# Optimization experiments

Hardware: AMD Instinct MI355X
Metric: run time of the kernel (lower is better)

## Reference

```python
import jax, jax.numpy as jnp
import numpy as np

N_NODES = 100000


def _gcn_conv(h, src, dst, norm, W, b, n):
    # linear transform then symmetric-normalized scatter-add aggregation
    hw = h @ W                                   # [N, out]
    msg = hw[src] * norm[:, None]                # [E+N, out] gathered messages
    out = jax.ops.segment_sum(msg, dst, num_segments=n)
    return out + b


def _self_loops_and_norm(edge_index, n):
    loop = jnp.arange(n, dtype=edge_index.dtype)
    src = jnp.concatenate([edge_index[0], loop])
    dst = jnp.concatenate([edge_index[1], loop])
    deg = jax.ops.segment_sum(jnp.ones_like(src, dtype=jnp.float32), dst, num_segments=n)
    dinv = jnp.where(deg > 0, jax.lax.rsqrt(jnp.maximum(deg, 1.0)), 0.0)
    norm = dinv[src] * dinv[dst]                 # D^-1/2 (A+I) D^-1/2 coefficients
    return src, dst, norm


def setup_inputs() -> dict:
    key = jax.random.key(0)
    k1, k2, k3, k4 = jax.random.split(key, 4)
    F_IN, H, C = 128, 64, 40
    x = jax.random.normal(k1, (N_NODES, F_IN), dtype=jnp.float32)
    edge_index = jax.random.randint(k2, (2, 3200000), 0, N_NODES, dtype=jnp.int64)
    s1 = 1.0 / np.sqrt(F_IN)
    s2 = 1.0 / np.sqrt(H)
    W1 = jax.random.uniform(k3, (F_IN, H), jnp.float32, -s1, s1)
    b1 = jnp.zeros((H,), jnp.float32)
    W2 = jax.random.uniform(k4, (H, C), jnp.float32, -s2, s2)
    b2 = jnp.zeros((C,), jnp.float32)
    return {"x": x, "edge_index": edge_index, "W1": W1, "b1": b1, "W2": W2, "b2": b2}


def reference(x, edge_index, W1, b1, W2, b2):
    n = x.shape[0]
    src, dst, norm = _self_loops_and_norm(edge_index, n)
    h = _gcn_conv(x, src, dst, norm, W1, b1, n)
    h = jax.nn.relu(h)
    # dropout(p=0.5) is identity in eval mode
    out = _gcn_conv(h, src, dst, norm, W2, b2, n)
    return jax.nn.log_softmax(out, axis=1)
```

## Files before the change

kernel.cpp:

```cpp
#include <hip/hip_runtime.h>
#include <math.h>

#define F_IN 128
#define HID  64
#define NCLS 40
#define PART_CHUNK 4096
#define CAP 4608
#define MAXNB 1024
#define ASTRIDE 132

typedef _Float16 half8 __attribute__((ext_vector_type(8)));
typedef _Float16 half2t __attribute__((ext_vector_type(2)));
typedef float floatx4 __attribute__((ext_vector_type(4)));

__device__ inline half8 ld_half8_u8(const _Float16* p) {
    union { uint2 u[2]; half8 h; } r;
    r.u[0] = *(const uint2*)p;
    r.u[1] = *(const uint2*)(p + 4);
    return r.h;
}

__global__ __launch_bounds__(256) void fused_part_gemm1(const int* __restrict__ src,
                                                        const int* __restrict__ dst,
                                                        int* __restrict__ bCur,
                                                        int* __restrict__ pkBuf,
                                                        int E, int NB, int nPart,
                                                        const float* __restrict__ x,
                                                        const float* __restrict__ W1,
                                                        _Float16* __restrict__ h1, int n) {
    __shared__ __align__(16) char smem[2 * 64 * ASTRIDE * 2];
    int tid = threadIdx.x;
    if ((int)blockIdx.x < nPart) {
        int* hcnt  = (int*)smem;
        int* hbase = (int*)smem + MAXNB;
        for (int i = tid; i < NB; i += 256) hcnt[i] = 0;
        __syncthreads();
        int e0 = blockIdx.x * PART_CHUNK;
        int s_[16], d_[16];
#pragma unroll
        for (int i = 0; i < 16; ++i) {
            int e = e0 + i * 256 + tid;
            if (e < E) {
                s_[i] = src[e]; d_[i] = dst[e];
                atomicAdd(&hcnt[d_[i] >> 7], 1);
            }
        }
        __syncthreads();
        for (int b = tid; b < NB; b += 256) {
            int c = hcnt[b];
            hbase[b] = c ? (b * CAP + atomicAdd(&bCur[b], c)) : 0;
            hcnt[b] = 0;
        }
        __syncthreads();
#pragma unroll
        for (int i = 0; i < 16; ++i) {
            int e = e0 + i * 256 + tid;
            if (e < E) {
                int b = d_[i] >> 7;
                int loc = atomicAdd(&hcnt[b], 1);
                pkBuf[hbase[b] + loc] = (s_[i] << 7) | (d_[i] & 127);
            }
        }
    } else {
        _Float16* Ah = (_Float16*)smem;
        _Float16* Wt = Ah + 64 * ASTRIDE;
        int node0 = ((int)blockIdx.x - nPart) * 64;
#pragma unroll
        for (int i = 0; i < 8; ++i) {
            int f = (i * 256 + tid) * 4;
            int m = f >> 7, k = f & 127;
            float4 v = (node0 + m < n) ? ((const float4*)(x + (size_t)(node0 + m) * F_IN))[k >> 2]
                                       : make_float4(0.f, 0.f, 0.f, 0.f);
            _Float16* p = &Ah[m * ASTRIDE + k];
            p[0] = (_Float16)v.x; p[1] = (_Float16)v.y; p[2] = (_Float16)v.z; p[3] = (_Float16)v.w;
        }
#pragma unroll
        for (int i = 0; i < 32; ++i) {
            int f = i * 256 + tid;
            int k = f >> 6, nn = f & 63;
            Wt[nn * ASTRIDE + k] = (_Float16)W1[f];
        }
        __syncthreads();
        int wave = tid >> 6, lane = tid & 63;
        int m0 = wave * 16;
        int col = lane & 15, quad = lane >> 4;
        floatx4 acc[4] = {{0,0,0,0},{0,0,0,0},{0,0,0,0},{0,0,0,0}};
#pragma unroll
        for (int kk = 0; kk < 4; ++kk) {
            int kbase = kk * 32 + quad * 8;
            half8 a = ld_half8_u8(&Ah[(m0 + col) * ASTRIDE + kbase]);
#pragma unroll
            for (int t = 0; t < 4; ++t) {
                half8 b = ld_half8_u8(&Wt[(t * 16 + col) * ASTRIDE + kbase]);
                acc[t] = __builtin_amdgcn_mfma_f32_16x16x32_f16(a, b, acc[t], 0, 0, 0);
            }
        }
#pragma unroll
        for (int t = 0; t < 4; ++t)
#pragma unroll
            for (int r = 0; r < 4; ++r) {
                int node = node0 + m0 + quad * 4 + r;
                if (node < n) h1[(size_t)node * HID + t * 16 + col] = (_Float16)acc[t][r];
            }
    }
}

__global__ __launch_bounds__(256) void scan_buckets(const int* __restrict__ bCur,
                                                    int* __restrict__ bBase, int NB, int E) {
    __shared__ int part[256];
    int tid = threadIdx.x;
    int v[4]; int sum = 0;
#pragma unroll
    for (int k = 0; k < 4; ++k) {
        int i = tid * 4 + k;
        v[k] = (i < NB) ? bCur[i] : 0;
        sum += v[k];
    }
    part[tid] = sum; __syncthreads();
    for (int off = 1; off < 256; off <<= 1) {
        int t = (tid >= off) ? part[tid - off] : 0;
        __syncthreads();
        part[tid] += t;
        __syncthreads();
    }
    int base = part[tid] - sum;
#pragma unroll
    for (int k = 0; k < 4; ++k) {
        int i = tid * 4 + k;
        if (i < NB) bBase[i] = base;
        base += v[k];
    }
    if (tid == 255) bBase[NB] = E;
}

__global__ __launch_bounds__(256) void bucket_finalize(const int* __restrict__ bCur,
                                                       const int* __restrict__ bBase,
                                                       const int* __restrict__ pkBuf,
                                                       int* __restrict__ ptr,
                                                       float* __restrict__ dinv,
                                                       int* __restrict__ sIdx, int n, int E) {
    __shared__ int cnt128[128];
    __shared__ int sc[128];
    __shared__ int cur[128];
    int b = blockIdx.x;
    int node0 = b << 7;
    int tid = threadIdx.x;
    if (tid < 128) cnt128[tid] = 0;
    __syncthreads();
    int beg = b * CAP, end = beg + bCur[b];
    int dbase = bBase[b];
    for (int j = beg + tid; j < end; j += 256)
        atomicAdd(&cnt128[pkBuf[j] & 127], 1);
    __syncthreads();
    int v = (tid < 128) ? cnt128[tid] : 0;
    if (tid < 128) sc[tid] = v;
    __syncthreads();
    for (int off = 1; off < 128; off <<= 1) {
        int t = (tid < 128 && tid >= off) ? sc[tid - off] : 0;
        __syncthreads();
        if (tid < 128) sc[tid] += t;
        __syncthreads();
    }
    if (tid < 128) {
        int node = node0 + tid;
        if (node < n) {
            int p = dbase + sc[tid] - v;
            ptr[node] = p;
            cur[tid] = p;
            dinv[node] = rsqrtf((float)v + 1.0f);
        }
    }
    if (tid == 0 && b == gridDim.x - 1) ptr[n] = E;
    __syncthreads();
    for (int j = beg + tid; j < end; j += 256) {
        int p = pkBuf[j];
        int pos = atomicAdd(&cur[p & 127], 1);
        sIdx[pos] = p >> 7;
    }
}

template<bool RELU>
__global__ __launch_bounds__(256) void gather4(const int* __restrict__ ptr,
                                               const int* __restrict__ sIdx,
                                               const float* __restrict__ dinv,
                                               const _Float16* __restrict__ hin,
                                               const float* __restrict__ bias,
                                               _Float16* __restrict__ hout, int n) {
    int tid = threadIdx.x, wave = tid >> 6, lane = tid & 63;
    int ng   = lane >> 4;
    int slot = (lane >> 3) & 1;
    int fq   = lane & 7;
    int node = blockIdx.x * 16 + wave * 4 + ng;
    bool valid = node < n;
    int nodeC = valid ? node : 0;
    int beg = ptr[nodeC];
    int end = valid ? ptr[nodeC + 1] : beg;
    float di = dinv[nodeC];
    float a0[8] = {0,0,0,0,0,0,0,0}, a1[8] = {0,0,0,0,0,0,0,0};

    if (slot == 0 && valid) {
        half8 v = *(const half8*)(hin + nodeC * HID + fq * 8);
        float w = di * di;
#pragma unroll
        for (int j = 0; j < 8; ++j) a0[j] = (float)v[j] * w;
    }
    for (int j0 = beg; j0 < end; j0 += 8) {
        int ja = j0 + slot, jb = j0 + 2 + slot, jc = j0 + 4 + slot, jd = j0 + 6 + slot;
        bool va = ja < end, vb = jb < end, vc = jc < end, vd = jd < end;
        int sa = sIdx[va ? ja : beg];
        int sb = sIdx[vb ? jb : beg];
        int sc_ = sIdx[vc ? jc : beg];
        int sd = sIdx[vd ? jd : beg];
        float wa = va ? dinv[sa] * di : 0.f;
        float wb = vb ? dinv[sb] * di : 0.f;
        float wc = vc ? dinv[sc_] * di : 0.f;
        float wd = vd ? dinv[sd] * di : 0.f;
        half8 ra = *(const half8*)(hin + sa * HID + fq * 8);
        half8 rb = *(const half8*)(hin + sb * HID + fq * 8);
        half8 rc = *(const half8*)(hin + sc_ * HID + fq * 8);
        half8 rd = *(const half8*)(hin + sd * HID + fq * 8);
#if __has_builtin(__builtin_amdgcn_fdot2)
        half2t wab = { (_Float16)wa, (_Float16)wb };
        half2t wcd = { (_Float16)wc, (_Float16)wd };
#pragma unroll
        for (int j = 0; j < 8; ++j) {
            half2t pab = { ra[j], rb[j] };
            half2t pcd = { rc[j], rd[j] };
            a0[j] = __builtin_amdgcn_fdot2(pab, wab, a0[j], false);
            a1[j] = __builtin_amdgcn_fdot2(pcd, wcd, a1[j], false);
        }
#else
#pragma unroll
        for (int j = 0; j < 8; ++j) {
            a0[j] = fmaf((float)ra[j], wa, a0[j]);
            a0[j] = fmaf((float)rb[j], wb, a0[j]);
            a1[j] = fmaf((float)rc[j], wc, a1[j]);
            a1[j] = fmaf((float)rd[j], wd, a1[j]);
        }
#endif
    }
#pragma unroll
    for (int j = 0; j < 8; ++j) {
        a0[j] += a1[j];
        a0[j] += __shfl_xor(a0[j], 8, 64);
    }
    if (slot == 0 && valid) {
        union { half8 h; uint4 u; } o;
#pragma unroll
        for (int j = 0; j < 8; ++j) {
            float v = a0[j];
            if (RELU) v = fmaxf(v + bias[fq * 8 + j], 0.f);
            o.h[j] = (_Float16)v;
        }
        *(uint4*)(hout + nodeC * HID + fq * 8) = o.u;
    }
}

#define GSTRIDE 72
__global__ __launch_bounds__(256) void gemm2_mfma_logsm(const _Float16* __restrict__ g,
                                                        const float* __restrict__ W2,
                                                        const float* __restrict__ b2,
                                                        float* __restrict__ out, int n) {
    __shared__ _Float16 gt[64 * GSTRIDE];
    __shared__ _Float16 wt[48 * GSTRIDE];
    int tid = threadIdx.x;
    int node0 = blockIdx.x * 64;
#pragma unroll
    for (int i = 0; i < 2; ++i) {
        int f = (i * 256 + tid) * 8;
        int m = f >> 6, k = f & 63;
        union { uint4 u; half8 h; } v;
        if (node0 + m < n) v.u = *(const uint4*)(g + (size_t)(node0 + m) * HID + k);
        else v.u = make_uint4(0, 0, 0, 0);
        *(uint4*)&gt[m * GSTRIDE + k] = v.u;
    }
#pragma unroll
    for (int i = 0; i < 12; ++i) {
        int f = i * 256 + tid;
        int c = f >> 6, k = f & 63;
        wt[c * GSTRIDE + k] = (c < NCLS) ? (_Float16)W2[k * NCLS + c] : (_Float16)0.f;
    }
    __syncthreads();

    int wave = tid >> 6, lane = tid & 63;
    int m0 = wave * 16;
    int col = lane & 15, quad = lane >> 4;
    floatx4 acc[3] = {{0,0,0,0},{0,0,0,0},{0,0,0,0}};
#pragma unroll
    for (int kk = 0; kk < 2; ++kk) {
        int kbase = kk * 32 + quad * 8;
        half8 a = *(const half8*)&gt[(m0 + col) * GSTRIDE + kbase];
#pragma unroll
        for (int t = 0; t < 3; ++t) {
            half8 b = *(const half8*)&wt[(t * 16 + col) * GSTRIDE + kbase];
            acc[t] = __builtin_amdgcn_mfma_f32_16x16x32_f16(a, b, acc[t], 0, 0, 0);
        }
    }
    float bb[3];
#pragma unroll
    for (int t = 0; t < 3; ++t) {
        int c = t * 16 + col;
        bb[t] = (c < NCLS) ? b2[c] : 0.f;
    }
#pragma unroll
    for (int r = 0; r < 4; ++r) {
        int node = node0 + m0 + quad * 4 + r;
        float v0 = acc[0][r] + bb[0];
        float v1 = acc[1][r] + bb[1];
        float v2 = (col < 8) ? acc[2][r] + bb[2] : -INFINITY;
        float m = fmaxf(fmaxf(v0, v1), v2);
#pragma unroll
        for (int off = 1; off < 16; off <<= 1) m = fmaxf(m, __shfl_xor(m, off, 64));
        float s = expf(v0 - m) + expf(v1 - m) + ((col < 8) ? expf(v2 - m) : 0.f);
#pragma unroll
        for (int off = 1; off < 16; off <<= 1) s += __shfl_xor(s, off, 64);
        float ls = logf(s);
        if (node < n) {
            float* op = out + (size_t)node * NCLS;
            op[col]      = v0 - m - ls;
            op[16 + col] = v1 - m - ls;
            if (col < 8) op[32 + col] = v2 - m - ls;
        }
    }
}

extern "C" void kernel_launch(void* const* d_in, const int* in_sizes, int n_in,
                              void* d_out, int out_size, void* d_ws, size_t ws_size,
                              hipStream_t stream) {
    const float* x  = (const float*)d_in[0];
    const int*   ei = (const int*)d_in[1];
    const float* W1 = (const float*)d_in[2];
    const float* b1 = (const float*)d_in[3];
    const float* W2 = (const float*)d_in[4];
    const float* b2 = (const float*)d_in[5];
    float* out = (float*)d_out;

    int n = in_sizes[0] / F_IN;
    int E = in_sizes[1] / 2;
    const int* src = ei;
    const int* dst = ei + E;
    int NB = (n + 127) >> 7;
    int nPart = (E + PART_CHUNK - 1) / PART_CHUNK;
    int nGemm1 = (n + 63) / 64;

    char* ws = (char*)d_ws;
    const size_t MB = 1024 * 1024;
    int*      bCur  = (int*)  (ws);
    int*      bBase = (int*)  (ws + 64 * 1024);
    int*      ptr   = (int*)  (ws + 128 * 1024);
    float*    dinv  = (float*)(ws + 1 * MB);
    int*      sIdx  = (int*)     (ws + 2 * MB);
    int*      pkBuf = (int*)     (ws + 15 * MB);
    _Float16* bufA  = (_Float16*)(ws + 30 * MB);
    _Float16* bufB  = (_Float16*)(ws + 43 * MB);

    hipMemsetAsync(bCur, 0, (size_t)NB * sizeof(int), stream);
    fused_part_gemm1<<<nPart + nGemm1, 256, 0, stream>>>(src, dst, bCur, pkBuf, E, NB, nPart,
                                                         x, W1, bufA, n);
    scan_buckets<<<1, 256, 0, stream>>>(bCur, bBase, NB, E);
    bucket_finalize<<<NB, 256, 0, stream>>>(bCur, bBase, pkBuf, ptr, dinv, sIdx, n, E);

    gather4<true ><<<(n + 15) / 16, 256, 0, stream>>>(ptr, sIdx, dinv, bufA, b1, bufB, n);
    gather4<false><<<(n + 15) / 16, 256, 0, stream>>>(ptr, sIdx, dinv, bufB, b1, bufA, n);
    gemm2_mfma_logsm<<<(n + 63) / 64, 256, 0, stream>>>(bufA, W2, b2, out, n);
}
```

Baseline: 329.8 us.

## Enlarge partition chunks and stage bucket finalize through shared memory

The partition blocks now handle 16384 edges each through a strided loop, so there are fewer blocks, fewer per-bucket global atomics, and larger contiguous runs per bucket. Because the edges are no longer kept in registers, src and dst are read from global memory twice. Bucket finalize now loads each bucket's packed edges into LDS once and scatters the source indices into an LDS staging array, then writes them to sIdx in coalesced order. This removes a second global read and the random global writes, at the cost of about 36KB of LDS per block, which may lower occupancy.

After: 352.8 us. +7.0%, slower.

```diff
diff --git a/kernel.cpp b/kernel.cpp
--- a/kernel.cpp
+++ b/kernel.cpp
@@ -4,7 +4,7 @@
 #define F_IN 128
 #define HID  64
 #define NCLS 40
-#define PART_CHUNK 4096
+#define PART_CHUNK 16384
 #define CAP 4608
 #define MAXNB 1024
 #define ASTRIDE 132
@@ -36,15 +36,9 @@
         for (int i = tid; i < NB; i += 256) hcnt[i] = 0;
         __syncthreads();
         int e0 = blockIdx.x * PART_CHUNK;
-        int s_[16], d_[16];
-#pragma unroll
-        for (int i = 0; i < 16; ++i) {
-            int e = e0 + i * 256 + tid;
-            if (e < E) {
-                s_[i] = src[e]; d_[i] = dst[e];
-                atomicAdd(&hcnt[d_[i] >> 7], 1);
-            }
-        }
+        int e1 = e0 + PART_CHUNK; if (e1 > E) e1 = E;
+        for (int e = e0 + tid; e < e1; e += 256)
+            atomicAdd(&hcnt[dst[e] >> 7], 1);
         __syncthreads();
         for (int b = tid; b < NB; b += 256) {
             int c = hcnt[b];
@@ -52,14 +46,11 @@
             hcnt[b] = 0;
         }
         __syncthreads();
-#pragma unroll
-        for (int i = 0; i < 16; ++i) {
-            int e = e0 + i * 256 + tid;
-            if (e < E) {
-                int b = d_[i] >> 7;
-                int loc = atomicAdd(&hcnt[b], 1);
-                pkBuf[hbase[b] + loc] = (s_[i] << 7) | (d_[i] & 127);
-            }
+        for (int e = e0 + tid; e < e1; e += 256) {
+            int d = dst[e];
+            int b = d >> 7;
+            int loc = atomicAdd(&hcnt[b], 1);
+            pkBuf[hbase[b] + loc] = (src[e] << 7) | (d & 127);
         }
     } else {
         _Float16* Ah = (_Float16*)smem;
@@ -142,15 +133,21 @@
     __shared__ int cnt128[128];
     __shared__ int sc[128];
     __shared__ int cur[128];
+    __shared__ int ebuf[CAP];
+    __shared__ int stage[CAP];
     int b = blockIdx.x;
     int node0 = b << 7;
     int tid = threadIdx.x;
     if (tid < 128) cnt128[tid] = 0;
     __syncthreads();
-    int beg = b * CAP, end = beg + bCur[b];
+    int beg = b * CAP;
+    int cnt = bCur[b];
     int dbase = bBase[b];
-    for (int j = beg + tid; j < end; j += 256)
-        atomicAdd(&cnt128[pkBuf[j] & 127], 1);
+    for (int j = tid; j < cnt; j += 256) {
+        int p = pkBuf[beg + j];
+        ebuf[j] = p;
+        atomicAdd(&cnt128[p & 127], 1);
+    }
     __syncthreads();
     int v = (tid < 128) ? cnt128[tid] : 0;
     if (tid < 128) sc[tid] = v;
@@ -162,21 +159,23 @@
         __syncthreads();
     }
     if (tid < 128) {
+        cur[tid] = sc[tid] - v;
         int node = node0 + tid;
         if (node < n) {
-            int p = dbase + sc[tid] - v;
-            ptr[node] = p;
-            cur[tid] = p;
+            ptr[node] = dbase + sc[tid] - v;
             dinv[node] = rsqrtf((float)v + 1.0f);
         }
     }
     if (tid == 0 && b == gridDim.x - 1) ptr[n] = E;
     __syncthreads();
-    for (int j = beg + tid; j < end; j += 256) {
-        int p = pkBuf[j];
+    for (int j = tid; j < cnt; j += 256) {
+        int p = ebuf[j];
         int pos = atomicAdd(&cur[p & 127], 1);
-        sIdx[pos] = p >> 7;
-    }
+        stage[pos] = p >> 7;
+    }
+    __syncthreads();
+    for (int j = tid; j < cnt; j += 256)
+        sIdx[dbase + j] = stage[j];
 }
 
 template<bool RELU>
```

## Split bucket counters per XCD and stage bucket CSR build in shared memory

Applied to the files above, without the earlier changes.

Bucket counters and edge-staging segments are split into 8 sub-buckets keyed by blockIdx mod 8, which likely tracks the XCD a block runs on. This is meant to reduce cross-die atomic contention on the global bucket cursors. bucket_finalize now loads all sub-segments into LDS once, scatters into an LDS staging array, and writes sIdx contiguously to make the global writes coalesced. It adds a larger shared memory footprint (about 37KB) that may lower occupancy. pkBuf now aliases bufB, and each per-XCD segment is capped at 768 entries, which could overflow on skewed inputs.

Result: faster. 320.9 us (-2.7%).

```diff
diff --git a/kernel.cpp b/kernel.cpp
--- a/kernel.cpp
+++ b/kernel.cpp
@@ -6,6 +6,7 @@
 #define NCLS 40
 #define PART_CHUNK 4096
 #define CAP 4608
+#define CAPX 768
 #define MAXNB 1024
 #define ASTRIDE 132
 
@@ -31,6 +32,7 @@
     __shared__ __align__(16) char smem[2 * 64 * ASTRIDE * 2];
     int tid = threadIdx.x;
     if ((int)blockIdx.x < nPart) {
+        int xcd = (int)blockIdx.x & 7;
         int* hcnt  = (int*)smem;
         int* hbase = (int*)smem + MAXNB;
         for (int i = tid; i < NB; i += 256) hcnt[i] = 0;
@@ -48,7 +50,7 @@
         __syncthreads();
         for (int b = tid; b < NB; b += 256) {
             int c = hcnt[b];
-            hbase[b] = c ? (b * CAP + atomicAdd(&bCur[b], c)) : 0;
+            hbase[b] = c ? ((b * 8 + xcd) * CAPX + atomicAdd(&bCur[b * 8 + xcd], c)) : 0;
             hcnt[b] = 0;
         }
         __syncthreads();
@@ -113,8 +115,13 @@
 #pragma unroll
     for (int k = 0; k < 4; ++k) {
         int i = tid * 4 + k;
-        v[k] = (i < NB) ? bCur[i] : 0;
-        sum += v[k];
+        int s = 0;
+        if (i < NB) {
+#pragma unroll
+            for (int x = 0; x < 8; ++x) s += bCur[i * 8 + x];
+        }
+        v[k] = s;
+        sum += s;
     }
     part[tid] = sum; __syncthreads();
     for (int off = 1; off < 256; off <<= 1) {
@@ -142,15 +149,31 @@
     __shared__ int cnt128[128];
     __shared__ int sc[128];
     __shared__ int cur[128];
+    __shared__ int segoff[9];
+    __shared__ int ebuf[CAP];
+    __shared__ int stage[CAP];
     int b = blockIdx.x;
     int node0 = b << 7;
     int tid = threadIdx.x;
     if (tid < 128) cnt128[tid] = 0;
-    __syncthreads();
-    int beg = b * CAP, end = beg + bCur[b];
+    if (tid == 0) {
+        int o = 0;
+#pragma unroll
+        for (int x = 0; x < 8; ++x) { segoff[x] = o; o += bCur[b * 8 + x]; }
+        segoff[8] = o;
+    }
+    __syncthreads();
+    int cnt = segoff[8];
     int dbase = bBase[b];
-    for (int j = beg + tid; j < end; j += 256)
-        atomicAdd(&cnt128[pkBuf[j] & 127], 1);
+    for (int x = 0; x < 8; ++x) {
+        int off = segoff[x], len = segoff[x + 1] - off;
+        const int* s = pkBuf + (size_t)(b * 8 + x) * CAPX;
+        for (int j = tid; j < len; j += 256) {
+            int p = s[j];
+            ebuf[off + j] = p;
+            atomicAdd(&cnt128[p & 127], 1);
+        }
+    }
     __syncthreads();
     int v = (tid < 128) ? cnt128[tid] : 0;
     if (tid < 128) sc[tid] = v;
@@ -162,21 +185,23 @@
         __syncthreads();
     }
     if (tid < 128) {
+        cur[tid] = sc[tid] - v;
         int node = node0 + tid;
         if (node < n) {
-            int p = dbase + sc[tid] - v;
-            ptr[node] = p;
-            cur[tid] = p;
+            ptr[node] = dbase + sc[tid] - v;
             dinv[node] = rsqrtf((float)v + 1.0f);
         }
     }
     if (tid == 0 && b == gridDim.x - 1) ptr[n] = E;
     __syncthreads();
-    for (int j = beg + tid; j < end; j += 256) {
-        int p = pkBuf[j];
+    for (int j = tid; j < cnt; j += 256) {
+        int p = ebuf[j];
         int pos = atomicAdd(&cur[p & 127], 1);
-        sIdx[pos] = p >> 7;
-    }
+        stage[pos] = p >> 7;
+    }
+    __syncthreads();
+    for (int j = tid; j < cnt; j += 256)
+        sIdx[dbase + j] = stage[j];
 }
 
 template<bool RELU>
@@ -350,11 +375,11 @@
     int*      ptr   = (int*)  (ws + 128 * 1024);
     float*    dinv  = (float*)(ws + 1 * MB);
     int*      sIdx  = (int*)     (ws + 2 * MB);
-    int*      pkBuf = (int*)     (ws + 15 * MB);
-    _Float16* bufA  = (_Float16*)(ws + 30 * MB);
-    _Float16* bufB  = (_Float16*)(ws + 43 * MB);
-
-    hipMemsetAsync(bCur, 0, (size_t)NB * sizeof(int), stream);
+    _Float16* bufA  = (_Float16*)(ws + 15 * MB);
+    int*      pkBuf = (int*)     (ws + 28 * MB);
+    _Float16* bufB  = (_Float16*)(ws + 28 * MB);
+
+    hipMemsetAsync(bCur, 0, (size_t)NB * 8 * sizeof(int), stream);
     fused_part_gemm1<<<nPart + nGemm1, 256, 0, stream>>>(src, dst, bCur, pkBuf, E, NB, nPart,
                                                          x, W1, bufA, n);
     scan_buckets<<<1, 256, 0, stream>>>(bCur, bBase, NB, E);
```
